# Kernel tuning notes

Measured on AMD Instinct MI355X. Metric: run time of the kernel, lower is better.

## Reference

```python
import jax, jax.numpy as jnp
import numpy as np

N = 2048      # num_nodes
B = 16        # batch
D_IN = 2      # input_dim per node
UNITS = 64    # rnn_units
F = D_IN + UNITS   # concat feature size = 66
M = 3         # num_matrices = (1 support + 1 adp hop)*K(=1) + 1 identity
E = N * 16    # sparse support edges (avg degree 16)


def _spmm(rows, cols, vals, x):
    # sparse support @ x, x: (N, K); equivalent of torch.sparse.mm
    return jax.ops.segment_sum(vals[:, None] * x[cols], rows, num_segments=N)


def _gconv(inputs, state, W, support_rows, support_cols, support_vals, adp):
    # inputs: (B, N*D_IN), state: (B, N*units) -> out: (B, N*out_dim)
    x = jnp.concatenate([inputs.reshape(B, N, -1), state.reshape(B, N, -1)], axis=2)  # (B,N,F)
    f = x.shape[2]
    x0 = x.transpose(1, 2, 0).reshape(N, f * B)                # (N, F*B)
    # diffusion step 1 over the single random_walk support
    x1 = _spmm(support_rows, support_cols, support_vals, x0)   # (N, F*B)
    # adaptive adjacency, k_hop=1 -> adp_lst = [adp], applied to x0
    x_temp = x0.reshape(N, f, B).transpose(2, 0, 1)            # (B,N,F)
    x2 = jnp.einsum('bnm,bmf->bnf', adp, x_temp)               # (B,N,F)
    x2 = x2.transpose(1, 2, 0).reshape(N, f * B)
    xs = jnp.stack([x0, x1, x2], axis=0)                       # (M,N,F*B)
    xs = xs.reshape(M, N, f, B).transpose(3, 1, 2, 0).reshape(B * N, f * M)
    out = xs @ W                                               # (B*N, out_dim)  (no bias: source never adds it)
    return out.reshape(B, N * W.shape[1])


def setup_inputs() -> dict:
    key = jax.random.key(0)
    ks = jax.random.split(key, 8)
    inputs = jax.random.normal(ks[0], (B, N * D_IN), dtype=jnp.float32)
    hx = jax.random.normal(ks[1], (B, N * UNITS), dtype=jnp.float32)
    adp = jax.random.uniform(ks[2], (B, N, N), dtype=jnp.float32) / N  # ~row-stochastic adaptive adj
    support_rows = jax.random.randint(ks[3], (E,), 0, N, dtype=jnp.int32)
    support_cols = jax.random.randint(ks[4], (E,), 0, N, dtype=jnp.int32)
    support_vals = jax.random.uniform(ks[5], (E,), dtype=jnp.float32) / 16.0
    W_ru = jax.random.normal(ks[6], (F * M, 2 * UNITS), dtype=jnp.float32) * 0.05
    W_c = jax.random.normal(ks[7], (F * M, UNITS), dtype=jnp.float32) * 0.05
    return dict(inputs=inputs, hx=hx, adp=adp, support_rows=support_rows,
                support_cols=support_cols, support_vals=support_vals,
                W_ru=W_ru, W_c=W_c, time_axis=0)


def reference(inputs, hx, adp, support_rows, support_cols, support_vals, W_ru, W_c, time_axis):
    # GRU with graph convolution gates (use_gc_for_ru=True, activation=tanh)
    ru = jax.nn.sigmoid(_gconv(inputs, hx, W_ru, support_rows, support_cols, support_vals, adp))
    ru = ru.reshape(B, N, 2 * UNITS)
    r = ru[..., :UNITS].reshape(B, N * UNITS)
    u = ru[..., UNITS:].reshape(B, N * UNITS)
    c = jnp.tanh(_gconv(inputs, r * hx, W_c, support_rows, support_cols, support_vals, adp))
    return u * hx + (1.0 - u) * c
```

## Files before the change

### kernel.cpp

```cpp
#include <hip/hip_runtime.h>
#include <cstdint>
#include <cstddef>

#define DN 2048
#define DB 16
#define DE 32768
#define FPAD 96

typedef __bf16 bf16x8 __attribute__((ext_vector_type(8)));
typedef __bf16 bf16x4 __attribute__((ext_vector_type(4)));
typedef float f32x4 __attribute__((ext_vector_type(4)));

__global__ __launch_bounds__(256) void prep_kernel(
    const float* __restrict__ inputs, const float* __restrict__ hx,
    const float* __restrict__ Wru, const float* __restrict__ Wc,
    __bf16* __restrict__ xcat1, __bf16* __restrict__ xcat2,
    __bf16* __restrict__ wtru, __bf16* __restrict__ wtc,
    int* __restrict__ cnt) {
  int idx = blockIdx.x * 256 + threadIdx.x;
  const int T1 = DB * DN * FPAD;
  if (idx < 2 * T1) {
    int which = idx >= T1 ? 1 : 0;
    int i = idx - which * T1;
    int f = i % FPAD;
    int bn = i / FPAD;
    int n = bn & (DN - 1);
    int b = bn >> 11;
    __bf16 v = (__bf16)0.0f;
    if (f < 2) v = (__bf16)inputs[(b << 12) + n * 2 + f];
    else if (f < 66 && !which) v = (__bf16)hx[((size_t)b << 17) + (n << 6) + (f - 2)];
    if (which) xcat2[i] = v; else xcat1[i] = v;
  } else {
    int j = idx - 2 * T1;
    if (j < 384 * FPAD) {
      int k = j % FPAD, o = j / FPAD;
      wtru[j] = (k < 66) ? (__bf16)Wru[(k * 3 + (o >> 7)) * 128 + (o & 127)] : (__bf16)0.0f;
    } else {
      j -= 384 * FPAD;
      if (j < 192 * FPAD) {
        int k = j % FPAD, o = j / FPAD;
        wtc[j] = (k < 66) ? (__bf16)Wc[(k * 3 + (o >> 6)) * 64 + (o & 63)] : (__bf16)0.0f;
      } else {
        j -= 192 * FPAD;
        if (j < DN) cnt[j] = 0;
      }
    }
  }
}

__global__ __launch_bounds__(512) void csr_count(const int* __restrict__ rows,
                                                 int* __restrict__ cnt) {
  int e = blockIdx.x * 512 + threadIdx.x;
  atomicAdd(&cnt[rows[e]], 1);
}

__global__ __launch_bounds__(1024) void csr_scan(const int* __restrict__ cnt,
                                                 int* __restrict__ csr_ptr,
                                                 int* __restrict__ off) {
  __shared__ int sa[DN];
  __shared__ int sb[DN];
  int t = threadIdx.x;
  int c0 = cnt[t], c1 = cnt[t + 1024];
  sa[t] = c0; sa[t + 1024] = c1;
  __syncthreads();
  int* src = sa; int* dst = sb;
  for (int o = 1; o < DN; o <<= 1) {
    for (int i = t; i < DN; i += 1024) {
      int v = src[i];
      if (i >= o) v += src[i - o];
      dst[i] = v;
    }
    __syncthreads();
    int* tmp = src; src = dst; dst = tmp;
  }
  int e0 = src[t] - c0;
  int e1 = src[t + 1024] - c1;
  csr_ptr[t] = e0; csr_ptr[t + 1024] = e1;
  off[t] = e0; off[t + 1024] = e1;
  if (t == 0) csr_ptr[DN] = DE;
}

__global__ __launch_bounds__(512) void csr_scatter(
    const int* __restrict__ rows, const int* __restrict__ cols,
    const float* __restrict__ vals, int* __restrict__ off,
    int* __restrict__ csr_col, float* __restrict__ csr_val) {
  int e = blockIdx.x * 512 + threadIdx.x;
  int r = rows[e];
  int p = atomicAdd(&off[r], 1);
  csr_col[p] = cols[e];
  csr_val[p] = vals[e];
}

template <int OD>
__global__ __launch_bounds__(256) void small_gemm(
    const __bf16* __restrict__ A, const __bf16* __restrict__ Bt,
    float* __restrict__ Y0, __bf16* __restrict__ y1b, __bf16* __restrict__ y2p) {
  __shared__ __attribute__((aligned(16))) __bf16 As[128 * 104];
  __shared__ __attribute__((aligned(16))) __bf16 Bs[64 * 104];
  int tid = threadIdx.x;
  int wave = tid >> 6, lane = tid & 63;
  int lrow = lane & 15, quad = lane >> 4;
  int r0 = blockIdx.x * 128;
  int c0 = blockIdx.y * 64;
  const uint4* gA = (const uint4*)(A + (size_t)r0 * FPAD);
  const uint4* gB = (const uint4*)(Bt + (size_t)c0 * FPAD);
  uint4* sA = (uint4*)As;
  uint4* sB = (uint4*)Bs;
#pragma unroll
  for (int i = 0; i < 6; ++i) {
    int s = i * 256 + tid;
    int r = s / 12, c4 = s % 12;
    sA[r * 13 + c4] = gA[r * 12 + c4];
  }
#pragma unroll
  for (int i = 0; i < 3; ++i) {
    int s = i * 256 + tid;
    int r = s / 12, c4 = s % 12;
    sB[r * 13 + c4] = gB[r * 12 + c4];
  }
  __syncthreads();
  int wm = wave >> 1, wn = wave & 1;
  f32x4 acc[4][2];
#pragma unroll
  for (int mt = 0; mt < 4; ++mt)
#pragma unroll
    for (int nt = 0; nt < 2; ++nt) acc[mt][nt] = (f32x4){0.f, 0.f, 0.f, 0.f};
#pragma unroll
  for (int kk = 0; kk < 3; ++kk) {
    bf16x8 af[4], bv[2];
#pragma unroll
    for (int mt = 0; mt < 4; ++mt)
      af[mt] = *(const bf16x8*)(As + (wm * 64 + mt * 16 + lrow) * 104 + kk * 32 + quad * 8);
#pragma unroll
    for (int nt = 0; nt < 2; ++nt)
      bv[nt] = *(const bf16x8*)(Bs + (wn * 32 + nt * 16 + lrow) * 104 + kk * 32 + quad * 8);
#pragma unroll
    for (int mt = 0; mt < 4; ++mt)
#pragma unroll
      for (int nt = 0; nt < 2; ++nt)
        acc[mt][nt] = __builtin_amdgcn_mfma_f32_16x16x32_bf16(af[mt], bv[nt], acc[mt][nt], 0, 0, 0);
  }
#pragma unroll
  for (int mt = 0; mt < 4; ++mt)
#pragma unroll
    for (int nt = 0; nt < 2; ++nt) {
      int col = c0 + wn * 32 + nt * 16 + lrow;
      int g = col >> ((OD == 128) ? 7 : 6);
      int oo = col & (OD - 1);
      int rowb = r0 + wm * 64 + mt * 16 + quad * 4;
      if (g == 2) {
        int bb = rowb >> 11;
        int n_ = rowb & 2047;
        bf16x4 v;
#pragma unroll
        for (int r = 0; r < 4; ++r) v[r] = (__bf16)acc[mt][nt][r];
        size_t off = ((((size_t)bb * (OD / 16) + (oo >> 4)) * 64 + (n_ >> 5)) * 4 +
                      ((n_ >> 3) & 3)) * 128 + (oo & 15) * 8 + (n_ & 7);
        *(bf16x4*)(y2p + off) = v;
      } else {
#pragma unroll
        for (int r = 0; r < 4; ++r) {
          int row = rowb + r;
          float v = acc[mt][nt][r];
          size_t oi = (size_t)row * OD + oo;
          if (g == 0) Y0[oi] = v;
          else y1b[oi] = (__bf16)v;
        }
      }
    }
}

template <int OD>
__global__ __launch_bounds__(256) void gather_pre(
    float* __restrict__ Y0, const __bf16* __restrict__ y1b,
    const int* __restrict__ csr_ptr, const int* __restrict__ csr_col,
    const float* __restrict__ csr_val) {
  constexpr int SH = (OD == 128) ? 7 : 6;
  int idx = blockIdx.x * 256 + threadIdx.x;
  int o = idx & (OD - 1);
  int bn = idx >> SH;
  int n = bn & (DN - 1);
  int b = bn >> 11;
  float acc = Y0[idx];
  int e1 = csr_ptr[n + 1];
  const __bf16* yb = y1b + ((size_t)b << 11) * OD;
  for (int e = csr_ptr[n]; e < e1; ++e)
    acc += csr_val[e] * (float)yb[(size_t)csr_col[e] * OD + o];
  Y0[idx] = acc;
}

template <int OD, bool IS_RU>
__global__ __launch_bounds__(256, 6) void adp_gemm(
    const float* __restrict__ adp, const __bf16* __restrict__ y2p,
    const float* __restrict__ pre, const float* __restrict__ hx,
    float* __restrict__ u_buf, __bf16* __restrict__ xcat2,
    float* __restrict__ outp) {
  constexpr int NT = OD / 64;
  int tid = threadIdx.x;
  int wave = tid >> 6, lane = tid & 63;
  int lrow = lane & 15, quad = lane >> 4;
  int hw = blockIdx.x;
  int swz = (hw & 7) * 256 + (hw >> 3);
  int b = swz >> 7;
  int row0 = (swz & 127) * 16;
  const float* Ap = adp + ((size_t)b * DN + row0 + lrow) * DN + quad * 8;
  const __bf16* Bq[NT];
#pragma unroll
  for (int nt = 0; nt < NT; ++nt) {
    int ob = wave * NT + nt;
    Bq[nt] = y2p + ((size_t)b * (OD / 16) + ob) * (64 * 512) + lane * 8;
  }

  f32x4 acc[NT];
#pragma unroll
  for (int nt = 0; nt < NT; ++nt) acc[nt] = (f32x4){0.f, 0.f, 0.f, 0.f};

#pragma unroll 1
  for (int c = 0; c < DN / 64; ++c) {
    bf16x8 bv[2][NT];
#pragma unroll
    for (int kk = 0; kk < 2; ++kk)
#pragma unroll
      for (int nt = 0; nt < NT; ++nt)
        bv[kk][nt] = *(const bf16x8*)(Bq[nt] + c * 1024 + kk * 512);
    const float* p_ = Ap + (size_t)c * 64;
    f32x4 a00 = *(const f32x4*)p_;
    f32x4 a01 = *(const f32x4*)(p_ + 4);
    f32x4 a10 = *(const f32x4*)(p_ + 32);
    f32x4 a11 = *(const f32x4*)(p_ + 36);
    bf16x8 af0, af1;
#pragma unroll
    for (int j = 0; j < 4; ++j) {
      af0[j] = (__bf16)a00[j]; af0[4 + j] = (__bf16)a01[j];
      af1[j] = (__bf16)a10[j]; af1[4 + j] = (__bf16)a11[j];
    }
#pragma unroll
    for (int nt = 0; nt < NT; ++nt)
      acc[nt] = __builtin_amdgcn_mfma_f32_16x16x32_bf16(af0, bv[0][nt], acc[nt], 0, 0, 0);
#pragma unroll
    for (int nt = 0; nt < NT; ++nt)
      acc[nt] = __builtin_amdgcn_mfma_f32_16x16x32_bf16(af1, bv[1][nt], acc[nt], 0, 0, 0);
  }

#pragma unroll
  for (int nt = 0; nt < NT; ++nt)
#pragma unroll
    for (int r = 0; r < 4; ++r) {
      int n = row0 + quad * 4 + r;
      int o = wave * (NT * 16) + nt * 16 + lrow;
      float g = acc[nt][r] + pre[((size_t)b * DN + n) * OD + o];
      if (IS_RU) {
        float s = 1.f / (1.f + __expf(-g));
        if (o < 64) {
          float hxv = hx[((size_t)b << 17) + n * 64 + o];
          xcat2[((size_t)b * DN + n) * FPAD + 2 + o] = (__bf16)(s * hxv);
        } else {
          u_buf[((size_t)b * DN + n) * 64 + (o - 64)] = s;
        }
      } else {
        float cval = 1.f - 2.f / (__expf(2.f * g) + 1.f);
        float u = u_buf[((size_t)b * DN + n) * 64 + o];
        float hxv = hx[((size_t)b << 17) + n * 64 + o];
        outp[((size_t)b << 17) + n * 64 + o] = u * hxv + (1.f - u) * cval;
      }
    }
}

extern "C" void kernel_launch(void* const* d_in, const int* in_sizes, int n_in,
                              void* d_out, int out_size, void* d_ws, size_t ws_size,
                              hipStream_t stream) {
  const float* inputs = (const float*)d_in[0];
  const float* hx     = (const float*)d_in[1];
  const float* adp    = (const float*)d_in[2];
  const int* srows    = (const int*)d_in[3];
  const int* scols    = (const int*)d_in[4];
  const float* svals  = (const float*)d_in[5];
  const float* Wru    = (const float*)d_in[6];
  const float* Wc     = (const float*)d_in[7];
  float* outp = (float*)d_out;

  char* w = (char*)d_ws;
  auto carve = [&](size_t bytes) -> char* {
    char* p = w;
    w += (bytes + 255) & ~(size_t)255;
    return p;
  };
  int*    csr_ptr = (int*)   carve((DN + 1) * sizeof(int));
  int*    csr_col = (int*)   carve(DE * sizeof(int));
  float*  csr_val = (float*) carve(DE * sizeof(float));
  int*    cnt     = (int*)   carve(DN * sizeof(int));
  int*    off     = (int*)   carve(DN * sizeof(int));
  __bf16* xcat1   = (__bf16*)carve((size_t)DB * DN * FPAD * 2);
  __bf16* xcat2   = (__bf16*)carve((size_t)DB * DN * FPAD * 2);
  __bf16* wtru    = (__bf16*)carve(384 * FPAD * 2);
  __bf16* wtc     = (__bf16*)carve(192 * FPAD * 2);
  float*  Y0      = (float*) carve((size_t)DB * DN * 128 * 4);
  __bf16* y1b     = (__bf16*)carve((size_t)DB * DN * 128 * 2);
  __bf16* y2b     = (__bf16*)carve((size_t)DB * DN * 128 * 2);
  __bf16* y2p     = (__bf16*)carve((size_t)DB * DN * 128 * 2);
  float*  u_buf   = (float*) carve((size_t)DB * DN * 64 * 4);
  (void)ws_size; (void)in_sizes; (void)n_in; (void)out_size; (void)y2b;

  prep_kernel<<<24800, 256, 0, stream>>>(inputs, hx, Wru, Wc, xcat1, xcat2,
                                         wtru, wtc, cnt);
  csr_count<<<64, 512, 0, stream>>>(srows, cnt);
  csr_scan<<<1, 1024, 0, stream>>>(cnt, csr_ptr, off);
  csr_scatter<<<64, 512, 0, stream>>>(srows, scols, svals, off, csr_col, csr_val);

  small_gemm<128><<<dim3(256, 6), 256, 0, stream>>>(xcat1, wtru, Y0, y1b, y2p);
  gather_pre<128><<<16384, 256, 0, stream>>>(Y0, y1b, csr_ptr, csr_col, csr_val);
  adp_gemm<128, true><<<2048, 256, 0, stream>>>(
      adp, y2p, Y0, hx, u_buf, xcat2, outp);

  small_gemm<64><<<dim3(256, 3), 256, 0, stream>>>(xcat2, wtc, Y0, y1b, y2p);
  gather_pre<64><<<8192, 256, 0, stream>>>(Y0, y1b, csr_ptr, csr_col, csr_val);
  adp_gemm<64, false><<<2048, 256, 0, stream>>>(
      adp, y2p, Y0, hx, u_buf, xcat2, outp);
}
```

Baseline: 801.1 us.

## Double-buffer adp GEMM tiles in LDS via async global_load_lds with 32-row blocks

The adaptive-adjacency GEMM now stages each 64-wide K chunk of the fp32 adp rows and the bf16 y2p tile into LDS with direct global-to-LDS loads, double-buffered so the next chunk loads while the current one feeds MFMA. Each block covers 32 rows instead of 16, with four waves in a 2x2 layout, which halves the grid and lets waves share the B tile through LDS rather than each reloading it from global memory. An XOR swizzle on the A tile is meant to avoid LDS bank conflicts. In exchange it adds barriers, hand-set vmcnt waits and more LDS per block, and lowers the occupancy hint from 6 to 4.

```diff
diff --git a/kernel.cpp b/kernel.cpp
--- a/kernel.cpp
+++ b/kernel.cpp
@@ -10,6 +10,11 @@
 typedef __bf16 bf16x8 __attribute__((ext_vector_type(8)));
 typedef __bf16 bf16x4 __attribute__((ext_vector_type(4)));
 typedef float f32x4 __attribute__((ext_vector_type(4)));
+
+#define GLOAD16(src, dst)                                              \
+  __builtin_amdgcn_global_load_lds(                                    \
+      (const __attribute__((address_space(1))) void*)(src),            \
+      (__attribute__((address_space(3))) void*)(dst), 16, 0, 0)
 
 __global__ __launch_bounds__(256) void prep_kernel(
     const float* __restrict__ inputs, const float* __restrict__ hx,
@@ -190,64 +195,104 @@
 }
 
 template <int OD, bool IS_RU>
-__global__ __launch_bounds__(256, 6) void adp_gemm(
+__global__ __launch_bounds__(256, 4) void adp_gemm(
     const float* __restrict__ adp, const __bf16* __restrict__ y2p,
     const float* __restrict__ pre, const float* __restrict__ hx,
     float* __restrict__ u_buf, __bf16* __restrict__ xcat2,
     float* __restrict__ outp) {
-  constexpr int NT = OD / 64;
+  constexpr int NT = OD / 32;
+  constexpr int NB = OD / 32;
+  constexpr int ABYTES = 32 * 256;
+  constexpr int BBYTES = OD * 128;
+  constexpr int BUFB = ABYTES + BBYTES;
+  __shared__ __attribute__((aligned(16))) char smem[2 * BUFB];
+
   int tid = threadIdx.x;
   int wave = tid >> 6, lane = tid & 63;
   int lrow = lane & 15, quad = lane >> 4;
+  int wm = wave >> 1, wn = wave & 1;
   int hw = blockIdx.x;
-  int swz = (hw & 7) * 256 + (hw >> 3);
-  int b = swz >> 7;
-  int row0 = (swz & 127) * 16;
-  const float* Ap = adp + ((size_t)b * DN + row0 + lrow) * DN + quad * 8;
-  const __bf16* Bq[NT];
-#pragma unroll
-  for (int nt = 0; nt < NT; ++nt) {
-    int ob = wave * NT + nt;
-    Bq[nt] = y2p + ((size_t)b * (OD / 16) + ob) * (64 * 512) + lane * 8;
-  }
+  int swz = (hw & 7) * 128 + (hw >> 3);
+  int b = swz >> 6;
+  int row0 = (swz & 63) * 32;
+  const float* Ab = adp + ((size_t)b * DN + row0) * DN;
+  const __bf16* Bbase = y2p + (size_t)b * (OD / 16) * 32768;
 
   f32x4 acc[NT];
 #pragma unroll
   for (int nt = 0; nt < NT; ++nt) acc[nt] = (f32x4){0.f, 0.f, 0.f, 0.f};
 
+  int Rrow = wm * 16 + lrow;
+
+  auto STAGE = [&](int buf, int c) {
+    char* base = smem + buf * BUFB;
+#pragma unroll
+    for (int i = 0; i < 2; ++i) {
+      int s = i * 256 + tid;
+      int r = s >> 4, h = s & 15;
+      int colf = ((((h >> 1) ^ (r & 7)) << 1) | (h & 1)) << 2;
+      const float* src = Ab + (size_t)r * DN + c * 64 + colf;
+      GLOAD16(src, base + s * 16);
+    }
+#pragma unroll
+    for (int i = 0; i < NB; ++i) {
+      int s = i * 256 + tid;
+      int ob = s >> 7, kk = (s >> 6) & 1, l = s & 63;
+      const __bf16* src = Bbase + (size_t)ob * 32768 + c * 1024 + kk * 512 + l * 8;
+      GLOAD16(src, base + ABYTES + s * 16);
+    }
+  };
+
+  auto COMPUTE = [&](int buf) {
+    const char* base = smem + buf * BUFB;
+    bf16x8 af[2];
+#pragma unroll
+    for (int kk = 0; kk < 2; ++kk) {
+      int chunk = (kk * 4 + quad) ^ (Rrow & 7);
+      const f32x4* pa = (const f32x4*)(base + Rrow * 256 + chunk * 32);
+      f32x4 a0 = pa[0], a1 = pa[1];
+#pragma unroll
+      for (int j = 0; j < 4; ++j) {
+        af[kk][j] = (__bf16)a0[j];
+        af[kk][4 + j] = (__bf16)a1[j];
+      }
+    }
+#pragma unroll
+    for (int kk = 0; kk < 2; ++kk)
+#pragma unroll
+      for (int nt = 0; nt < NT; ++nt) {
+        int ob = wn * NT + nt;
+        bf16x8 bv = *(const bf16x8*)(base + ABYTES + ob * 2048 + kk * 1024 + lane * 16);
+        acc[nt] = __builtin_amdgcn_mfma_f32_16x16x32_bf16(af[kk], bv, acc[nt], 0, 0, 0);
+      }
+  };
+
+  STAGE(0, 0);
 #pragma unroll 1
-  for (int c = 0; c < DN / 64; ++c) {
-    bf16x8 bv[2][NT];
-#pragma unroll
-    for (int kk = 0; kk < 2; ++kk)
-#pragma unroll
-      for (int nt = 0; nt < NT; ++nt)
-        bv[kk][nt] = *(const bf16x8*)(Bq[nt] + c * 1024 + kk * 512);
-    const float* p_ = Ap + (size_t)c * 64;
-    f32x4 a00 = *(const f32x4*)p_;
-    f32x4 a01 = *(const f32x4*)(p_ + 4);
-    f32x4 a10 = *(const f32x4*)(p_ + 32);
-    f32x4 a11 = *(const f32x4*)(p_ + 36);
-    bf16x8 af0, af1;
-#pragma unroll
-    for (int j = 0; j < 4; ++j) {
-      af0[j] = (__bf16)a00[j]; af0[4 + j] = (__bf16)a01[j];
-      af1[j] = (__bf16)a10[j]; af1[4 + j] = (__bf16)a11[j];
-    }
-#pragma unroll
-    for (int nt = 0; nt < NT; ++nt)
-      acc[nt] = __builtin_amdgcn_mfma_f32_16x16x32_bf16(af0, bv[0][nt], acc[nt], 0, 0, 0);
-#pragma unroll
-    for (int nt = 0; nt < NT; ++nt)
-      acc[nt] = __builtin_amdgcn_mfma_f32_16x16x32_bf16(af1, bv[1][nt], acc[nt], 0, 0, 0);
-  }
+  for (int c = 0; c < DN / 64 - 1; ++c) {
+    STAGE((c + 1) & 1, c + 1);
+    if constexpr (OD == 128) {
+      asm volatile("s_waitcnt vmcnt(6)" ::: "memory");
+    } else {
+      asm volatile("s_waitcnt vmcnt(4)" ::: "memory");
+    }
+    __builtin_amdgcn_sched_barrier(0);
+    __builtin_amdgcn_s_barrier();
+    __builtin_amdgcn_sched_barrier(0);
+    COMPUTE(c & 1);
+    __builtin_amdgcn_s_barrier();
+  }
+  asm volatile("s_waitcnt vmcnt(0)" ::: "memory");
+  __builtin_amdgcn_sched_barrier(0);
+  __builtin_amdgcn_s_barrier();
+  COMPUTE(1);
 
 #pragma unroll
   for (int nt = 0; nt < NT; ++nt)
 #pragma unroll
     for (int r = 0; r < 4; ++r) {
-      int n = row0 + quad * 4 + r;
-      int o = wave * (NT * 16) + nt * 16 + lrow;
+      int n = row0 + wm * 16 + quad * 4 + r;
+      int o = wn * (NT * 16) + nt * 16 + lrow;
       float g = acc[nt][r] + pre[((size_t)b * DN + n) * OD + o];
       if (IS_RU) {
         float s = 1.f / (1.f + __expf(-g));
@@ -309,11 +354,11 @@
 
   small_gemm<128><<<dim3(256, 6), 256, 0, stream>>>(xcat1, wtru, Y0, y1b, y2p);
   gather_pre<128><<<16384, 256, 0, stream>>>(Y0, y1b, csr_ptr, csr_col, csr_val);
-  adp_gemm<128, true><<<2048, 256, 0, stream>>>(
+  adp_gemm<128, true><<<1024, 256, 0, stream>>>(
       adp, y2p, Y0, hx, u_buf, xcat2, outp);
 
   small_gemm<64><<<dim3(256, 3), 256, 0, stream>>>(xcat2, wtc, Y0, y1b, y2p);
   gather_pre<64><<<8192, 256, 0, stream>>>(Y0, y1b, csr_ptr, csr_col, csr_val);
-  adp_gemm<64, false><<<2048, 256, 0, stream>>>(
+  adp_gemm<64, false><<<1024, 256, 0, stream>>>(
       adp, y2p, Y0, hx, u_buf, xcat2, outp);
 }
```

New measurement: 692.8 us. -13.5%, faster.
